# Kernel tuning notes

Hardware: AMD Instinct MI355X
Metric: run time of the kernel (lower is better)

## Reference

```python
import jax, jax.numpy as jnp
import numpy as np

B, S, D_IN = 4, 2048, 1024
EMBED, H = 1024, 16
HD = EMBED // H  # 64


def setup_inputs() -> dict:
    key = jax.random.key(0)
    k1, k2, k3 = jax.random.split(key, 3)
    x = jax.random.normal(k1, (B, S, D_IN), dtype=jnp.float32)
    # xavier_uniform for torch Linear weight [out, in]
    lim_qkv = float(np.sqrt(6.0 / (D_IN + 3 * EMBED)))
    W_qkv = jax.random.uniform(k2, (3 * EMBED, D_IN), minval=-lim_qkv, maxval=lim_qkv, dtype=jnp.float32)
    b_qkv = jnp.zeros((3 * EMBED,), dtype=jnp.float32)
    lim_o = float(np.sqrt(6.0 / (EMBED + EMBED)))
    W_out = jax.random.uniform(k3, (EMBED, EMBED), minval=-lim_o, maxval=lim_o, dtype=jnp.float32)
    b_out = jnp.zeros((EMBED,), dtype=jnp.float32)
    return {"x": x, "W_qkv": W_qkv, "b_qkv": b_qkv, "W_out": W_out, "b_out": b_out}


def reference(x, W_qkv, b_qkv, W_out, b_out):
    b, s, _ = x.shape
    qkv = x @ W_qkv.T + b_qkv                      # [b, s, 3*embed]
    # einops 'b s (h c d) -> c b h s d': fused dim groups as (h, 3, d)
    qkv = qkv.reshape(b, s, H, 3, HD)
    qkv = jnp.transpose(qkv, (3, 0, 2, 1, 4))      # [3, b, h, s, d]
    q, k, v = qkv[0], qkv[1], qkv[2]
    scale = 1.0 / jnp.sqrt(jnp.asarray(HD, dtype=q.dtype))
    logits = jnp.einsum('bhqd,bhkd->bhqk', q, k) * scale
    attn = jax.nn.softmax(logits, axis=-1)
    vals = jnp.einsum('bhqk,bhkd->bhqd', attn, v)  # [b, h, s, d]
    vals = jnp.transpose(vals, (0, 2, 1, 3)).reshape(b, s, EMBED)
    return vals @ W_out.T + b_out
```

## Files before the change

### kernel.cpp

```cpp
#include <hip/hip_runtime.h>
#include <hip/hip_bf16.h>
#include <stdint.h>

#define B_   4
#define S_   2048
#define DIN  1024
#define EMB  1024
#define H_   16
#define HD_  64
#define TOK  (B_*S_)
#define NQKV 3072

using bf16  = __hip_bfloat16;
using f32x4 = __attribute__((ext_vector_type(4))) float;
using f32x16 = __attribute__((ext_vector_type(16))) float;
using s16x8 = __attribute__((ext_vector_type(8))) short;
using bf16x8 = __attribute__((ext_vector_type(8))) __bf16;

__device__ __forceinline__ f32x4 mfma16(s16x8 a, s16x8 b, f32x4 c) {
  return __builtin_amdgcn_mfma_f32_16x16x32_bf16(
      __builtin_bit_cast(bf16x8, a), __builtin_bit_cast(bf16x8, b), c, 0, 0, 0);
}
__device__ __forceinline__ f32x16 mfma32(s16x8 a, s16x8 b, f32x16 c) {
  return __builtin_amdgcn_mfma_f32_32x32x16_bf16(
      __builtin_bit_cast(bf16x8, a), __builtin_bit_cast(bf16x8, b), c, 0, 0, 0);
}

__device__ __forceinline__ void gload_lds16(const void* g, void* l) {
  __builtin_amdgcn_global_load_lds(
      (const __attribute__((address_space(1))) uint32_t*)g,
      (__attribute__((address_space(3))) uint32_t*)l, 16, 0, 0);
}

__device__ __forceinline__ uint32_t cvtpk_bf16(float lo, float hi) {
  uint32_t r;
  asm("v_cvt_pk_bf16_f32 %0, %1, %2" : "=v"(r) : "v"(lo), "v"(hi));
  return r;
}
__device__ __forceinline__ void plswap32(uint32_t &a, uint32_t &b) {
  asm("v_permlane32_swap_b32 %0, %1" : "+v"(a), "+v"(b));
}

union U8 { s16x8 v; bf16 b[8]; };
union PaU { uint32_t w[4]; s16x8 v; };

__global__ __launch_bounds__(256) void cvt_all(const float* __restrict__ x,
                                               const float* __restrict__ wqkv,
                                               const float* __restrict__ wout,
                                               bf16* __restrict__ xb,
                                               bf16* __restrict__ wqkvb,
                                               bf16* __restrict__ woutb) {
  int b = blockIdx.x;
  const float* in; bf16* out; int base;
  if (b < 4096)      { in = x;    out = xb;    base = b; }
  else if (b < 5632) { in = wqkv; out = wqkvb; base = b - 4096; }
  else               { in = wout; out = woutb; base = b - 5632; }
  int i = (base * 256 + (int)threadIdx.x) * 8;
  float4 a = *(const float4*)(in + i);
  float4 c = *(const float4*)(in + i + 4);
  U8 u;
  u.b[0] = __float2bfloat16(a.x); u.b[1] = __float2bfloat16(a.y);
  u.b[2] = __float2bfloat16(a.z); u.b[3] = __float2bfloat16(a.w);
  u.b[4] = __float2bfloat16(c.x); u.b[5] = __float2bfloat16(c.y);
  u.b[6] = __float2bfloat16(c.z); u.b[7] = __float2bfloat16(c.w);
  *(s16x8*)(out + i) = u.v;
}

template<int MODE>
__global__ __launch_bounds__(256) void gemm_bt(
    const bf16* __restrict__ A, const bf16* __restrict__ Bw,
    const float* __restrict__ bias,
    bf16* __restrict__ outQK, bf16* __restrict__ outV,
    float* __restrict__ outF, int N, int K)
{
  const int tid  = threadIdx.x;
  const int lane = tid & 63;
  const int w    = tid >> 6;
  const int wm   = w >> 1, wn = w & 1;
  const int bn0  = blockIdx.x * 128;
  const int bm0  = blockIdx.y * 128;

  __shared__ __align__(16) bf16 As[128 * 64];
  __shared__ __align__(16) bf16 Bs[128 * 64];

  f32x4 acc[4][4];
  const f32x4 zero = {0.f, 0.f, 0.f, 0.f};
  for (int mt = 0; mt < 4; ++mt)
    for (int nt = 0; nt < 4; ++nt) acc[mt][nt] = zero;

  for (int kt = 0; kt < K; kt += 64) {
    for (int i = 0; i < 4; ++i) {
      int c   = i * 256 + tid;
      int row = c >> 3, p = c & 7;
      int sc  = p ^ (row & 7);
      gload_lds16(A + (size_t)(bm0 + row) * K + kt + sc * 8, (char*)As + c * 16);
      gload_lds16(Bw + (size_t)(bn0 + row) * K + kt + sc * 8, (char*)Bs + c * 16);
    }
    __syncthreads();

    s16x8 af[4][2], bfr[4][2];
    for (int mt = 0; mt < 4; ++mt)
      for (int kk = 0; kk < 2; ++kk) {
        int row  = wm * 64 + mt * 16 + (lane & 15);
        int byte = row * 128 + (((kk * 4 + (lane >> 4)) ^ (row & 7)) << 4);
        af[mt][kk] = *(const s16x8*)((const char*)As + byte);
      }
    for (int nt = 0; nt < 4; ++nt)
      for (int kk = 0; kk < 2; ++kk) {
        int row  = wn * 64 + nt * 16 + (lane & 15);
        int byte = row * 128 + (((kk * 4 + (lane >> 4)) ^ (row & 7)) << 4);
        bfr[nt][kk] = *(const s16x8*)((const char*)Bs + byte);
      }
    for (int kk = 0; kk < 2; ++kk)
      for (int mt = 0; mt < 4; ++mt)
        for (int nt = 0; nt < 4; ++nt)
          acc[mt][nt] = mfma16(af[mt][kk], bfr[nt][kk], acc[mt][nt]);
    __syncthreads();
  }

  const int col_l = lane & 15;
  const int rgrp  = lane >> 4;
  for (int mt = 0; mt < 4; ++mt)
    for (int nt = 0; nt < 4; ++nt) {
      int n0  = bn0 + wn * 64 + nt * 16;
      int col = n0 + col_l;
      float bv = bias[col];
      if (MODE == 0) {
        int h = col / 192, rem = col % 192;
        int cc = rem / 64, d = rem % 64;
        for (int r = 0; r < 4; ++r) {
          int row = bm0 + wm * 64 + mt * 16 + rgrp * 4 + r;
          bf16 bvv = __float2bfloat16(acc[mt][nt][r] + bv);
          if (cc == 2) {
            int bb = row >> 11, s = row & 2047;
            outV[(((size_t)bb * H_ + h) * HD_ + d) * S_ + s] = bvv;
          } else {
            outQK[(size_t)row * NQKV + col] = bvv;
          }
        }
      } else {
        for (int r = 0; r < 4; ++r) {
          int row = bm0 + wm * 64 + mt * 16 + rgrp * 4 + r;
          outF[(size_t)row * EMB + col] = acc[mt][nt][r] + bv;
        }
      }
    }
}

__global__ __launch_bounds__(512, 1) void attn2(const bf16* __restrict__ qkvb,
                                                const bf16* __restrict__ vb,
                                                bf16* __restrict__ ob)
{
  const int tid = threadIdx.x, lane = tid & 63, w = tid >> 6;
  const int hi = lane >> 5, l31 = lane & 31;
  const int f  = blockIdx.x;
  const int bh = (f & 7) | ((f >> 5) << 3);
  const int qt = (f >> 3) & 3;
  const int bb = bh >> 4, h = bh & 15;
  const int q0 = qt * 512;
  const size_t tokbase = (size_t)bb * S_;

  __shared__ __align__(16) char KsB[2][8 * 1040];
  __shared__ __align__(16) char VtsB[2][8 * 1040];

  s16x8 qf0[4], qf1[4];
  {
    const int qrow = q0 + w * 64 + l31;
    const bf16* qp = qkvb + (tokbase + qrow) * NQKV + h * 192 + hi * 8;
    #pragma unroll
    for (int ks = 0; ks < 4; ++ks) {
      U8 u; u.v = *(const s16x8*)(qp + ks * 16);
      #pragma unroll
      for (int j = 0; j < 8; ++j)
        u.b[j] = __float2bfloat16(__bfloat162float(u.b[j]) * 0.18033688011112042f);
      qf0[ks] = u.v;
    }
    const bf16* qp1 = qp + (size_t)32 * NQKV;
    #pragma unroll
    for (int ks = 0; ks < 4; ++ks) {
      U8 u; u.v = *(const s16x8*)(qp1 + ks * 16);
      #pragma unroll
      for (int j = 0; j < 8; ++j)
        u.b[j] = __float2bfloat16(__bfloat162float(u.b[j]) * 0.18033688011112042f);
      qf1[ks] = u.v;
    }
  }

  f32x16 zero16;
  #pragma unroll
  for (int i = 0; i < 16; ++i) zero16[i] = 0.f;
  f32x16 oA0 = zero16, oB0 = zero16, oA1 = zero16, oB1 = zero16;
  f32x16 nm0 = zero16, nm1 = zero16;
  float l00 = 0.f, l01 = 0.f;

  const bf16* Kbase = qkvb + tokbase * NQKV + h * 192 + 64;
  const bf16* Vbase = vb + (size_t)bh * HD_ * S_;

  const int srow = tid >> 3, sp = tid & 7;
  const bf16* kSrc = Kbase + (size_t)srow * NQKV + sp * 8;
  const bf16* vSrc = Vbase + (size_t)srow * S_ + sp * 8;
  const int   sByte = sp * 1040 + srow * 16;

  s16x8 kreg, vreg;
  auto LOAD = [&](int t) {
    kreg = *(const s16x8*)(kSrc + (size_t)t * 64 * NQKV);
    vreg = *(const s16x8*)(vSrc + (size_t)t * 64);
  };
  auto WRITE = [&](int b) {
    *(s16x8*)(KsB[b] + sByte) = kreg;
    *(s16x8*)(VtsB[b] + sByte) = vreg;
  };

  LOAD(0);
  WRITE(0);
  __syncthreads();

  int cur = 0;
  for (int t = 0; t < S_ / 64; ++t) {
    if (t < S_ / 64 - 1) LOAD(t + 1);

    f32x16 pA0, pB0, pA1, pB1;
    #pragma unroll
    for (int ks = 0; ks < 4; ++ks) {
      const char* kb = KsB[cur] + (2 * ks + hi) * 1040;
      s16x8 klo = *(const s16x8*)(kb + l31 * 16);
      s16x8 khi = *(const s16x8*)(kb + 512 + l31 * 16);
      pA0 = mfma32(klo, qf0[ks], ks == 0 ? nm0 : pA0);
      pB0 = mfma32(khi, qf0[ks], ks == 0 ? nm0 : pB0);
      pA1 = mfma32(klo, qf1[ks], ks == 0 ? nm1 : pA1);
      pB1 = mfma32(khi, qf1[ks], ks == 0 ? nm1 : pB1);
    }

    float mx0[8], mx1[8];
    #pragma unroll
    for (int i = 0; i < 8; ++i) {
      mx0[i] = fmaxf(fmaxf(pA0[i], pA0[i + 8]), fmaxf(pB0[i], pB0[i + 8]));
      mx1[i] = fmaxf(fmaxf(pA1[i], pA1[i + 8]), fmaxf(pB1[i], pB1[i + 8]));
    }
    float pmax0 = fmaxf(fmaxf(fmaxf(mx0[0], mx0[4]), fmaxf(mx0[1], mx0[5])),
                        fmaxf(fmaxf(mx0[2], mx0[6]), fmaxf(mx0[3], mx0[7])));
    float pmax1 = fmaxf(fmaxf(fmaxf(mx1[0], mx1[4]), fmaxf(mx1[1], mx1[5])),
                        fmaxf(fmaxf(mx1[2], mx1[6]), fmaxf(mx1[3], mx1[7])));
    pmax0 = fmaxf(pmax0, __shfl_xor(pmax0, 32));
    pmax1 = fmaxf(pmax1, __shfl_xor(pmax1, 32));

    if (__any(fmaxf(pmax0, pmax1) > 11.0f)) {
      float al0 = __builtin_amdgcn_exp2f(-pmax0);
      float al1 = __builtin_amdgcn_exp2f(-pmax1);
      l00 *= al0; l01 *= al1;
      #pragma unroll
      for (int r = 0; r < 16; ++r) {
        int crow = (r & 3) + 8 * (r >> 2) + 4 * hi;
        float a0 = __shfl(al0, crow), a1 = __shfl(al1, crow);
        oA0[r] *= a0; oB0[r] *= a0;
        oA1[r] *= a1; oB1[r] *= a1;
      }
      #pragma unroll
      for (int r = 0; r < 16; ++r) {
        pA0[r] -= pmax0; pB0[r] -= pmax0;
        pA1[r] -= pmax1; pB1[r] -= pmax1;
      }
      #pragma unroll
      for (int i = 0; i < 16; ++i) { nm0[i] -= pmax0; nm1[i] -= pmax1; }
    }

    #pragma unroll
    for (int r = 0; r < 16; ++r) {
      pA0[r] = __builtin_amdgcn_exp2f(pA0[r]);
      pB0[r] = __builtin_amdgcn_exp2f(pB0[r]);
      pA1[r] = __builtin_amdgcn_exp2f(pA1[r]);
      pB1[r] = __builtin_amdgcn_exp2f(pB1[r]);
    }
    {
      float s80[8], s81[8];
      #pragma unroll
      for (int i = 0; i < 8; ++i) {
        s80[i] = (pA0[i] + pA0[i + 8]) + (pB0[i] + pB0[i + 8]);
        s81[i] = (pA1[i] + pA1[i + 8]) + (pB1[i] + pB1[i + 8]);
      }
      l00 += ((s80[0] + s80[1]) + (s80[2] + s80[3])) +
             ((s80[4] + s80[5]) + (s80[6] + s80[7]));
      l01 += ((s81[0] + s81[1]) + (s81[2] + s81[3])) +
             ((s81[4] + s81[5]) + (s81[6] + s81[7]));
    }

    PaU pa0[4], pa1[4];
    #pragma unroll
    for (int s = 0; s < 4; ++s) {
      const int sub = s & 1;
      {
        const f32x16 &ph = (s < 2) ? pA0 : pB0;
        uint32_t L0 = cvtpk_bf16(ph[8 * sub + 0], ph[8 * sub + 1]);
        uint32_t L1 = cvtpk_bf16(ph[8 * sub + 2], ph[8 * sub + 3]);
        uint32_t H0 = cvtpk_bf16(ph[8 * sub + 4], ph[8 * sub + 5]);
        uint32_t H1 = cvtpk_bf16(ph[8 * sub + 6], ph[8 * sub + 7]);
        plswap32(L0, H0); plswap32(L1, H1);
        pa0[s].w[0] = L0; pa0[s].w[1] = L1; pa0[s].w[2] = H0; pa0[s].w[3] = H1;
      }
      {
        const f32x16 &ph = (s < 2) ? pA1 : pB1;
        uint32_t L0 = cvtpk_bf16(ph[8 * sub + 0], ph[8 * sub + 1]);
        uint32_t L1 = cvtpk_bf16(ph[8 * sub + 2], ph[8 * sub + 3]);
        uint32_t H0 = cvtpk_bf16(ph[8 * sub + 4], ph[8 * sub + 5]);
        uint32_t H1 = cvtpk_bf16(ph[8 * sub + 6], ph[8 * sub + 7]);
        plswap32(L0, H0); plswap32(L1, H1);
        pa1[s].w[0] = L0; pa1[s].w[1] = L1; pa1[s].w[2] = H0; pa1[s].w[3] = H1;
      }
    }

    #pragma unroll
    for (int s = 0; s < 4; ++s) {
      const char* vbp = VtsB[cur] + (2 * s + hi) * 1040;
      s16x8 vlo = *(const s16x8*)(vbp + l31 * 16);
      s16x8 vhi = *(const s16x8*)(vbp + 512 + l31 * 16);
      oA0 = mfma32(pa0[s].v, vlo, oA0);
      oB0 = mfma32(pa0[s].v, vhi, oB0);
      oA1 = mfma32(pa1[s].v, vlo, oA1);
      oB1 = mfma32(pa1[s].v, vhi, oB1);
    }

    if (t < S_ / 64 - 1) WRITE(cur ^ 1);
    __syncthreads();
    cur ^= 1;
  }

  float l0t0 = l00 + __shfl_xor(l00, 32);
  float l0t1 = l01 + __shfl_xor(l01, 32);
  float inv0 = 1.0f / l0t0, inv1 = 1.0f / l0t1;
  #pragma unroll
  for (int r = 0; r < 16; ++r) {
    int q = (r & 3) + 8 * (r >> 2) + 4 * hi;
    float ir0 = __shfl(inv0, q), ir1 = __shfl(inv1, q);
    int qrow = q0 + w * 64 + q;
    bf16* op0 = ob + (tokbase + qrow) * EMB + h * 64 + l31;
    op0[0]  = __float2bfloat16(oA0[r] * ir0);
    op0[32] = __float2bfloat16(oB0[r] * ir0);
    bf16* op1 = op0 + (size_t)32 * EMB;
    op1[0]  = __float2bfloat16(oA1[r] * ir1);
    op1[32] = __float2bfloat16(oB1[r] * ir1);
  }
}

extern "C" void kernel_launch(void* const* d_in, const int* in_sizes, int n_in,
                              void* d_out, int out_size, void* d_ws, size_t ws_size,
                              hipStream_t stream) {
  const float* x    = (const float*)d_in[0];
  const float* Wqkv = (const float*)d_in[1];
  const float* bqkv = (const float*)d_in[2];
  const float* Wout = (const float*)d_in[3];
  const float* bout = (const float*)d_in[4];
  float* out = (float*)d_out;

  char* ws = (char*)d_ws;
  bf16* xb    = (bf16*)(ws);
  bf16* wqkvb = (bf16*)(ws + 16777216);
  bf16* woutb = (bf16*)(ws + 23068672);
  bf16* qkvb  = (bf16*)(ws + 25165824);
  bf16* vb    = (bf16*)(ws + 75497472);
  bf16* ob    = xb;

  cvt_all<<<dim3(6144), 256, 0, stream>>>(x, Wqkv, Wout, xb, wqkvb, woutb);

  gemm_bt<0><<<dim3(NQKV / 128, TOK / 128), 256, 0, stream>>>(
      xb, wqkvb, bqkv, qkvb, vb, nullptr, NQKV, DIN);

  attn2<<<dim3(256), 512, 0, stream>>>(qkvb, vb, ob);

  gemm_bt<1><<<dim3(EMB / 128, TOK / 128), 256, 0, stream>>>(
      ob, woutb, bout, nullptr, nullptr, out, EMB, EMB);
}
```

Before: 195.9 us.

## Replace QKV projection GEMM with 256x256-tile 8-wave pipelined kernel

Adds a new GEMM kernel with 256x256 output tiles, 512 threads and 128 KB of dynamic LDS. It double-buffers K-tiles loaded straight into LDS and splits each K step into four quadrant phases that interleave LDS reads, next-tile global loads and MFMA bursts under raised wave priority. The QKV projection now uses it in place of the 128x128 kernel. The aim is more data reuse per tile and better overlap of memory with matrix math, at the cost of fewer blocks (384 on the device) and one-block-per-CU occupancy.

```diff
diff --git a/kernel.cpp b/kernel.cpp
--- a/kernel.cpp
+++ b/kernel.cpp
@@ -147,6 +147,126 @@
     }
 }
 
+#define VMF(n) { asm volatile("s_waitcnt vmcnt(" #n ")" ::: "memory"); \
+                 __builtin_amdgcn_sched_barrier(0); }
+#define BARX() __builtin_amdgcn_s_barrier()
+
+template<int MODE>
+__global__ __launch_bounds__(512, 1) void gemm8(
+    const bf16* __restrict__ A, const bf16* __restrict__ Bw,
+    const float* __restrict__ bias,
+    bf16* __restrict__ outQK, bf16* __restrict__ outV,
+    float* __restrict__ outF, int N, int K)
+{
+  extern __shared__ char lds8[];
+  const int tid = threadIdx.x, lane = tid & 63, w = tid >> 6;
+  const int wm = w >> 2, wn = w & 3;
+  const int bn0 = blockIdx.x * 256, bm0 = blockIdx.y * 256;
+  const int NT = K >> 6;
+
+  const bf16* aSrc[2][2]; const bf16* bSrc[2][2];
+  #pragma unroll
+  for (int i = 0; i < 2; ++i) {
+    int j = i * 512 + tid, rlh = j >> 3, p = j & 7;
+    #pragma unroll
+    for (int h = 0; h < 2; ++h) {
+      int r = (rlh & 63) + h * 64 + (rlh >> 6) * 128;
+      aSrc[i][h] = A + (size_t)(bm0 + r) * K + (p ^ (r & 7)) * 8;
+      int n = (rlh >> 5) * 64 + h * 32 + (rlh & 31);
+      bSrc[i][h] = Bw + (size_t)(bn0 + n) * K + (p ^ (n & 7)) * 8;
+    }
+  }
+  const int dst16 = tid * 16;
+
+#define SA8(buf,h,kt) { _Pragma("unroll") for (int i = 0; i < 2; ++i) \
+    gload_lds16(aSrc[i][h] + (kt) * 64, lds8 + ((buf)*2+(h))*16384 + i*8192 + dst16); }
+#define SB8(buf,h,kt) { _Pragma("unroll") for (int i = 0; i < 2; ++i) \
+    gload_lds16(bSrc[i][h] + (kt) * 64, lds8 + 65536 + ((buf)*2+(h))*16384 + i*8192 + dst16); }
+
+  s16x8 af[4][2], bfv[2][2][2];
+#define LDA8(buf,mh) { _Pragma("unroll") for (int mf = 0; mf < 4; ++mf) { \
+    int r = wm*128 + (mh)*64 + mf*16 + (lane & 15); \
+    int rlh = (r & 63) + ((r >> 7) & 1) * 64; \
+    _Pragma("unroll") for (int kk = 0; kk < 2; ++kk) \
+      af[mf][kk] = *(const s16x8*)(lds8 + ((buf)*2+(mh))*16384 + rlh*128 + \
+                                   (((kk*4 + (lane>>4)) ^ (r & 7)) << 4)); } }
+#define LDB8(buf,nh) { _Pragma("unroll") for (int nf = 0; nf < 2; ++nf) { \
+    int n = wn*64 + (nh)*32 + nf*16 + (lane & 15); \
+    int rlh = wn*32 + nf*16 + (lane & 15); \
+    _Pragma("unroll") for (int kk = 0; kk < 2; ++kk) \
+      bfv[nh][nf][kk] = *(const s16x8*)(lds8 + 65536 + ((buf)*2+(nh))*16384 + \
+                                        rlh*128 + (((kk*4 + (lane>>4)) ^ (n & 7)) << 4)); } }
+#define QUAD8(mh,nh) { _Pragma("unroll") for (int kk = 0; kk < 2; ++kk) \
+    _Pragma("unroll") for (int mf = 0; mf < 4; ++mf) \
+    _Pragma("unroll") for (int nf = 0; nf < 2; ++nf) \
+      acc[(mh)*4+mf][(nh)*2+nf] = mfma16(af[mf][kk], bfv[nh][nf][kk], \
+                                         acc[(mh)*4+mf][(nh)*2+nf]); }
+
+  f32x4 acc[8][4];
+  const f32x4 zero = {0.f, 0.f, 0.f, 0.f};
+  #pragma unroll
+  for (int mq = 0; mq < 8; ++mq)
+    #pragma unroll
+    for (int nq = 0; nq < 4; ++nq) acc[mq][nq] = zero;
+
+  SA8(0,0,0); SB8(0,0,0); SA8(0,1,0); SB8(0,1,0);
+  SA8(1,0,1); SB8(1,0,1);
+  VMF(8); BARX();
+
+  for (int t = 0; t < NT; ++t) {
+    const int buf = t & 1, nxt = buf ^ 1;
+    LDA8(buf,0); LDB8(buf,0);
+    if (t + 1 < NT) SA8(nxt,1,t+1);
+    BARX();
+    __builtin_amdgcn_s_setprio(1); QUAD8(0,0); __builtin_amdgcn_s_setprio(0);
+    VMF(6); BARX();
+    LDB8(buf,1);
+    if (t + 1 < NT) SB8(nxt,1,t+1);
+    BARX();
+    __builtin_amdgcn_s_setprio(1); QUAD8(0,1); __builtin_amdgcn_s_setprio(0);
+    BARX();
+    LDA8(buf,1);
+    if (t + 2 < NT) SA8(buf,0,t+2);
+    BARX();
+    __builtin_amdgcn_s_setprio(1); QUAD8(1,0); __builtin_amdgcn_s_setprio(0);
+    BARX();
+    if (t + 2 < NT) SB8(buf,0,t+2);
+    BARX();
+    __builtin_amdgcn_s_setprio(1); QUAD8(1,1); __builtin_amdgcn_s_setprio(0);
+    VMF(8); BARX();
+  }
+
+  const int col_l = lane & 15, rgrp = lane >> 4;
+  #pragma unroll
+  for (int mq = 0; mq < 8; ++mq)
+    #pragma unroll
+    for (int nq = 0; nq < 4; ++nq) {
+      int col = bn0 + wn * 64 + nq * 16 + col_l;
+      float bv = bias[col];
+      if (MODE == 0) {
+        int h = col / 192, rem = col % 192;
+        int cc = rem / 64, d = rem % 64;
+        #pragma unroll
+        for (int r = 0; r < 4; ++r) {
+          int row = bm0 + wm * 128 + mq * 16 + rgrp * 4 + r;
+          bf16 bvv = __float2bfloat16(acc[mq][nq][r] + bv);
+          if (cc == 2) {
+            int bb = row >> 11, s = row & 2047;
+            outV[(((size_t)bb * H_ + h) * HD_ + d) * S_ + s] = bvv;
+          } else {
+            outQK[(size_t)row * NQKV + col] = bvv;
+          }
+        }
+      } else {
+        #pragma unroll
+        for (int r = 0; r < 4; ++r) {
+          int row = bm0 + wm * 128 + mq * 16 + rgrp * 4 + r;
+          outF[(size_t)row * EMB + col] = acc[mq][nq][r] + bv;
+        }
+      }
+    }
+}
+
 __global__ __launch_bounds__(512, 1) void attn2(const bf16* __restrict__ qkvb,
                                                 const bf16* __restrict__ vb,
                                                 bf16* __restrict__ ob)
@@ -359,9 +479,12 @@
   bf16* vb    = (bf16*)(ws + 75497472);
   bf16* ob    = xb;
 
+  (void)hipFuncSetAttribute((const void*)gemm8<0>,
+                            hipFuncAttributeMaxDynamicSharedMemorySize, 131072);
+
   cvt_all<<<dim3(6144), 256, 0, stream>>>(x, Wqkv, Wout, xb, wqkvb, woutb);
 
-  gemm_bt<0><<<dim3(NQKV / 128, TOK / 128), 256, 0, stream>>>(
+  gemm8<0><<<dim3(NQKV / 256, TOK / 256), 512, 131072, stream>>>(
       xb, wqkvb, bqkv, qkvb, vb, nullptr, NQKV, DIN);
 
   attn2<<<dim3(256), 512, 0, stream>>>(qkvb, vb, ob);
```

After: 203.1 us. 3.7% more time.
